# Performance work log

Hardware: AMD Instinct MI355X
Metric: run time of the kernel (lower is better)

Reference implementation:

```python
import jax, jax.numpy as jnp
import numpy as np

N_EMBD = 1024
N_HEAD = 16
HEAD = N_EMBD // N_HEAD


def setup_inputs() -> dict:
    key = jax.random.key(0)
    ks = jax.random.split(key, 5)
    B, T = 2, 2048
    s = 1.0 / np.sqrt(N_EMBD)
    return {
        "x": jax.random.normal(ks[0], (B, T, N_EMBD), dtype=jnp.float32),
        "w_attn": jax.random.normal(ks[1], (N_EMBD, 3 * N_EMBD), dtype=jnp.float32) * s,
        "b_attn": jnp.zeros((3 * N_EMBD,), dtype=jnp.float32),
        "w_proj": jax.random.normal(ks[2], (N_EMBD, N_EMBD), dtype=jnp.float32) * s,
        "b_proj": jnp.zeros((N_EMBD,), dtype=jnp.float32),
    }


def reference(x, w_attn, b_attn, w_proj, b_proj):
    B, T, C = x.shape
    qkv = x @ w_attn + b_attn                      # [B,T,3C]
    q, k, v = jnp.split(qkv, 3, axis=-1)
    def heads(t):
        return t.reshape(B, T, N_HEAD, HEAD).transpose(0, 2, 1, 3)  # [B,H,T,D]
    q, k, v = heads(q), heads(k), heads(v)
    scale = 1.0 / np.sqrt(HEAD).astype(np.float32)
    scores = jnp.einsum('bhqd,bhkd->bhqk', q, k) * scale
    causal = jnp.tril(jnp.ones((T, T), dtype=bool))
    scores = jnp.where(causal, scores, -jnp.inf)
    attn = jax.nn.softmax(scores, axis=-1)
    out = jnp.einsum('bhqk,bhkd->bhqd', attn, v)   # [B,H,T,D]
    out = out.transpose(0, 2, 1, 3).reshape(B, T, C)
    return out @ w_proj + b_proj
```

## Files before the change

### kernel.cpp

```cpp
#include <hip/hip_runtime.h>
#include <stdint.h>

#define N_EMBD 1024
#define N_HEADv 16
#define HEADv 64
#define Bv 2
#define Tv 2048
#define BT (Bv*Tv)
#define C3 (3*N_EMBD)

typedef __attribute__((ext_vector_type(8))) short bf16x8;
typedef __attribute__((ext_vector_type(4))) float f32x4;

typedef __attribute__((address_space(3))) uint32_t lds_u32;
typedef const __attribute__((address_space(1))) uint32_t glb_u32;

__device__ __forceinline__ void gload_lds16(const void* g, void* l){
  __builtin_amdgcn_global_load_lds((glb_u32*)g, (lds_u32*)l, 16, 0, 0);
}

__device__ __forceinline__ unsigned short f2bf(float f){
  union { float f; uint32_t u; } v; v.f = f;
  uint32_t u = v.u;
  uint32_t r = u + 0x7FFFu + ((u>>16)&1u);
  return (unsigned short)(r>>16);
}
__device__ __forceinline__ uint32_t f2bf_fast(float f){
  union { float f; uint32_t u; } v; v.f = f;
  return (v.u + 0x8000u) >> 16;
}
__device__ __forceinline__ float bf2f(unsigned short s){
  union { uint32_t u; float f; } v; v.u = ((uint32_t)s)<<16; return v.f;
}

__global__ void k_cvt_bf16(const float* __restrict__ in, unsigned short* __restrict__ out, long n){
  long i = ((long)blockIdx.x*blockDim.x + threadIdx.x)*8;
  if(i >= n) return;
  float4 a = *reinterpret_cast<const float4*>(in+i);
  float4 b = *reinterpret_cast<const float4*>(in+i+4);
  union { int4 v; unsigned short s[8]; } o;
  o.s[0]=f2bf(a.x); o.s[1]=f2bf(a.y); o.s[2]=f2bf(a.z); o.s[3]=f2bf(a.w);
  o.s[4]=f2bf(b.x); o.s[5]=f2bf(b.y); o.s[6]=f2bf(b.z); o.s[7]=f2bf(b.w);
  *reinterpret_cast<int4*>(out+i) = o.v;
}

__global__ void k_transpose_bf16(const float* __restrict__ in, unsigned short* __restrict__ out, int K, int N){
  __shared__ float tile[64][65];
  int n0 = blockIdx.x*64, k0 = blockIdx.y*64;
  int t = threadIdx.x;
  #pragma unroll
  for(int p=0;p<4;p++){
    int row = (t>>4) + p*16;
    int col4 = (t&15)*4;
    float4 v = *reinterpret_cast<const float4*>(&in[(size_t)(k0+row)*N + n0 + col4]);
    tile[row][col4+0]=v.x; tile[row][col4+1]=v.y; tile[row][col4+2]=v.z; tile[row][col4+3]=v.w;
  }
  __syncthreads();
  #pragma unroll
  for(int p=0;p<4;p++){
    int nrow = (t>>4) + p*16;
    int kc = (t&15)*4;
    ushort4 o;
    o.x = f2bf(tile[kc+0][nrow]);
    o.y = f2bf(tile[kc+1][nrow]);
    o.z = f2bf(tile[kc+2][nrow]);
    o.w = f2bf(tile[kc+3][nrow]);
    *reinterpret_cast<ushort4*>(&out[(size_t)(n0+nrow)*K + k0 + kc]) = o;
  }
}

template<int MODE>
__global__ __launch_bounds__(256) void k_gemm(
    const unsigned short* __restrict__ A,
    const unsigned short* __restrict__ Bt,
    const float* __restrict__ bias,
    void* __restrict__ Cout,
    int M, int N, int K)
{
  const int BK=64;
  const int TSZ=128*BK;
  __shared__ unsigned short As[2*TSZ];
  __shared__ unsigned short Bs[2*TSZ];
  int m0 = blockIdx.y*128, n0 = blockIdx.x*128;
  int t = threadIdx.x, lane = t&63, wid = t>>6;
  int wm = (wid>>1)*64, wn = (wid&1)*64;
  int g = lane>>4, r16 = lane&15;
  int rl  = lane>>3;
  int cle = (((lane&7) ^ rl) * 8);
  int rsw = r16 & 7;
  f32x4 acc[4][4] = {};

  #pragma unroll
  for(int c=0;c<4;c++){
    int rb = wid*32 + c*8;
    gload_lds16(&A [(size_t)(m0+rb+rl)*K + cle], &As[rb*BK]);
    gload_lds16(&Bt[(size_t)(n0+rb+rl)*K + cle], &Bs[rb*BK]);
  }
  __syncthreads();

  const int NIT = K/BK;
  for(int it=0; it<NIT; ++it){
    int cur = it & 1;
    if(it+1 < NIT){
      int k0 = (it+1)*BK;
      int nxt = (cur^1)*TSZ;
      #pragma unroll
      for(int c=0;c<4;c++){
        int rb = wid*32 + c*8;
        gload_lds16(&A [(size_t)(m0+rb+rl)*K + k0 + cle], &As[nxt + rb*BK]);
        gload_lds16(&Bt[(size_t)(n0+rb+rl)*K + k0 + cle], &Bs[nxt + rb*BK]);
      }
    }
    const unsigned short* Ab = &As[cur*TSZ];
    const unsigned short* Bb = &Bs[cur*TSZ];
    bf16x8 af[2][4], bfr[2][4];
    #pragma unroll
    for(int ks=0;ks<2;ks++){
      #pragma unroll
      for(int mi=0;mi<4;mi++)
        af[ks][mi]  = *reinterpret_cast<const bf16x8*>(&Ab[(wm+mi*16+r16)*BK + (((ks*4+g)^rsw)*8)]);
      #pragma unroll
      for(int ni=0;ni<4;ni++)
        bfr[ks][ni] = *reinterpret_cast<const bf16x8*>(&Bb[(wn+ni*16+r16)*BK + (((ks*4+g)^rsw)*8)]);
    }
    __builtin_amdgcn_s_setprio(1);
    #pragma unroll
    for(int ks=0;ks<2;ks++)
      #pragma unroll
      for(int mi=0;mi<4;mi++)
        #pragma unroll
        for(int ni=0;ni<4;ni++){
          if(MODE==0)
            acc[mi][ni] = __builtin_amdgcn_mfma_f32_16x16x32_bf16(af[ks][mi], bfr[ks][ni], acc[mi][ni], 0,0,0);
          else
            acc[mi][ni] = __builtin_amdgcn_mfma_f32_16x16x32_bf16(bfr[ks][ni], af[ks][mi], acc[mi][ni], 0,0,0);
        }
    __builtin_amdgcn_s_setprio(0);
    __syncthreads();
  }

  if(MODE==0){
    int which = (n0+wn)>>10;
    int h = ((n0+wn)&1023)>>6;
    int bb = m0>>11;
    int tt0 = (m0&2047) + wm;
    unsigned short* base = (unsigned short*)Cout;
    if(which < 2){
      float scale = (which==0) ? 0.18033688f : 1.0f;
      unsigned short* dst = base + (size_t)which*BT*N_EMBD
                          + (((size_t)bb*N_HEADv + h)*Tv + tt0)*HEADv;
      #pragma unroll
      for(int ni=0;ni<4;ni++){
        float bv = bias[n0+wn+ni*16+r16];
        int d = ni*16 + r16;
        #pragma unroll
        for(int mi=0;mi<4;mi++)
          #pragma unroll
          for(int reg=0;reg<4;reg++){
            int tt = mi*16 + g*4 + reg;
            dst[(size_t)tt*HEADv + d] = f2bf((acc[mi][ni][reg] + bv)*scale);
          }
      }
    } else {
      unsigned short* dst = base + 2ll*BT*N_EMBD
                          + (((size_t)bb*N_HEADv + h)*HEADv)*Tv + tt0;
      #pragma unroll
      for(int ni=0;ni<4;ni++){
        float bv = bias[n0+wn+ni*16+r16];
        int d = ni*16 + r16;
        #pragma unroll
        for(int mi=0;mi<4;mi++)
          #pragma unroll
          for(int reg=0;reg<4;reg++){
            int tt = mi*16 + g*4 + reg;
            dst[(size_t)d*Tv + tt] = f2bf(acc[mi][ni][reg] + bv);
          }
      }
    }
  } else {
    float* out = (float*)Cout;
    #pragma unroll
    for(int mi=0;mi<4;mi++){
      int m = m0+wm+mi*16+r16;
      #pragma unroll
      for(int ni=0;ni<4;ni++){
        int n = n0+wn+ni*16+g*4;
        float4 b4 = *reinterpret_cast<const float4*>(&bias[n]);
        float4 o4;
        o4.x = acc[mi][ni][0] + b4.x;
        o4.y = acc[mi][ni][1] + b4.y;
        o4.z = acc[mi][ni][2] + b4.z;
        o4.w = acc[mi][ni][3] + b4.w;
        *reinterpret_cast<float4*>(&out[(size_t)m*N + n]) = o4;
      }
    }
  }
}

__global__ __launch_bounds__(256) void k_attn(
    const unsigned short* __restrict__ QKV,
    unsigned short* __restrict__ O,
    unsigned short* __restrict__ partO,
    float2* __restrict__ stats)
{
  __shared__ unsigned short Ks[2][64][64];
  __shared__ unsigned short Vs[2][64][64];
  __shared__ unsigned short Ps[4][16][64];
  int blk = blockIdx.x;
  int bh = blk & 31;
  int j  = blk >> 5;
  int qt, kt0, ktN; bool single;
  if(j < 16)      { qt = 16+j;  kt0 = 0;  ktN = 16;    single = false; }
  else if(j < 32) { qt = 47-j;  kt0 = 16; ktN = qt+1;  single = false; }
  else            { qt = 47-j;  kt0 = 0;  ktN = qt+1;  single = true;  }

  int t = threadIdx.x, lane=t&63, wid=t>>6;
  int g = lane>>4, r16 = lane&15;
  const unsigned short* Qp  = QKV + (size_t)bh*Tv*HEADv;
  const unsigned short* Kp  = QKV + (size_t)BT*N_EMBD + (size_t)bh*Tv*HEADv;
  const unsigned short* Vtp = QKV + 2ll*BT*N_EMBD + (size_t)bh*HEADv*Tv;
  int q0 = qt*64 + wid*16;

  bf16x8 aq[2];
  #pragma unroll
  for(int kb=0;kb<2;kb++)
    aq[kb] = *reinterpret_cast<const bf16x8*>(&Qp[(size_t)(q0+r16)*HEADv + kb*32 + g*8]);

  const short ONE = (short)0x3F80;
  const bf16x8 ones8 = {ONE,ONE,ONE,ONE,ONE,ONE,ONE,ONE};

  f32x4 oacc[4] = {};
  f32x4 lacc = {};
  float m2 = 6.0f;

  int r0 = t>>3, c0 = (t&7)*8;
  int r1 = r0 + 32;
  int sw0 = c0 ^ ((r0&7)<<3);
  int sw1 = c0 ^ ((r1&7)<<3);
  int rsw = (r16&7)<<3;

  int4 kc0, kc1, vc0, vc1;
  kc0 = *reinterpret_cast<const int4*>(&Kp [(size_t)(kt0*64+r0)*HEADv + c0]);
  kc1 = *reinterpret_cast<const int4*>(&Kp [(size_t)(kt0*64+r1)*HEADv + c0]);
  vc0 = *reinterpret_cast<const int4*>(&Vtp[(size_t)r0*Tv + kt0*64 + c0]);
  vc1 = *reinterpret_cast<const int4*>(&Vtp[(size_t)r1*Tv + kt0*64 + c0]);
  *reinterpret_cast<int4*>(&Ks[0][r0][sw0]) = kc0;
  *reinterpret_cast<int4*>(&Ks[0][r1][sw1]) = kc1;
  *reinterpret_cast<int4*>(&Vs[0][r0][sw0]) = vc0;
  *reinterpret_cast<int4*>(&Vs[0][r1][sw1]) = vc1;
  if(ktN - kt0 > 1){
    kc0 = *reinterpret_cast<const int4*>(&Kp [(size_t)((kt0+1)*64+r0)*HEADv + c0]);
    kc1 = *reinterpret_cast<const int4*>(&Kp [(size_t)((kt0+1)*64+r1)*HEADv + c0]);
    vc0 = *reinterpret_cast<const int4*>(&Vtp[(size_t)r0*Tv + (kt0+1)*64 + c0]);
    vc1 = *reinterpret_cast<const int4*>(&Vtp[(size_t)r1*Tv + (kt0+1)*64 + c0]);
  }
  __syncthreads();

  for(int kt=kt0; kt<ktN; ++kt){
    int cur = kt & 1;
    if(kt+1 < ktN){
      *reinterpret_cast<int4*>(&Ks[cur^1][r0][sw0]) = kc0;
      *reinterpret_cast<int4*>(&Ks[cur^1][r1][sw1]) = kc1;
      *reinterpret_cast<int4*>(&Vs[cur^1][r0][sw0]) = vc0;
      *reinterpret_cast<int4*>(&Vs[cur^1][r1][sw1]) = vc1;
      if(kt+2 < ktN){
        kc0 = *reinterpret_cast<const int4*>(&Kp [(size_t)((kt+2)*64+r0)*HEADv + c0]);
        kc1 = *reinterpret_cast<const int4*>(&Kp [(size_t)((kt+2)*64+r1)*HEADv + c0]);
        vc0 = *reinterpret_cast<const int4*>(&Vtp[(size_t)r0*Tv + (kt+2)*64 + c0]);
        vc1 = *reinterpret_cast<const int4*>(&Vtp[(size_t)r1*Tv + (kt+2)*64 + c0]);
      }
    }

    f32x4 sacc[4];
    __builtin_amdgcn_s_setprio(1);
    #pragma unroll
    for(int nb=0;nb<4;nb++){
      sacc[nb] = (f32x4){0.f,0.f,0.f,0.f};
      #pragma unroll
      for(int kb=0;kb<2;kb++){
        bf16x8 bk = *reinterpret_cast<const bf16x8*>(&Ks[cur][nb*16+r16][(kb*32+g*8) ^ rsw]);
        sacc[nb] = __builtin_amdgcn_mfma_f32_16x16x32_bf16(bk, aq[kb], sacc[nb],0,0,0);
      }
    }
    __builtin_amdgcn_s_setprio(0);

    bool diag = (kt == qt);
    float sv[4][4], pv[4][4];
    #pragma unroll
    for(int nb=0;nb<4;nb++)
      #pragma unroll
      for(int reg=0;reg<4;reg++){
        float s = sacc[nb][reg];
        if(diag){
          int keyin = nb*16 + g*4 + reg;
          if(keyin > wid*16 + r16) s = -1e30f;
        }
        sv[nb][reg] = s;
      }
    #pragma unroll
    for(int nb=0;nb<4;nb++)
      #pragma unroll
      for(int reg=0;reg<4;reg++)
        pv[nb][reg] = __builtin_amdgcn_exp2f(sv[nb][reg] - m2);

    float mxnb[4];
    #pragma unroll
    for(int nb=0;nb<4;nb++)
      mxnb[nb] = fmaxf(fmaxf(sv[nb][0],sv[nb][1]), fmaxf(sv[nb][2],sv[nb][3]));
    float mx = fmaxf(fmaxf(mxnb[0],mxnb[1]), fmaxf(mxnb[2],mxnb[3]));
    mx = fmaxf(mx, __shfl_xor(mx, 16, 64));
    mx = fmaxf(mx, __shfl_xor(mx, 32, 64));

    if(!__all(mx - m2 <= 11.5f)){
      float mn = fmaxf(m2, mx);
      float alpha = __builtin_amdgcn_exp2f(m2 - mn);
      lacc[0]*=alpha; lacc[1]*=alpha; lacc[2]*=alpha; lacc[3]*=alpha;
      #pragma unroll
      for(int nb=0;nb<4;nb++)
        #pragma unroll
        for(int reg=0;reg<4;reg++) oacc[nb][reg] *= alpha;
      m2 = mn;
      #pragma unroll
      for(int nb=0;nb<4;nb++)
        #pragma unroll
        for(int reg=0;reg<4;reg++)
          pv[nb][reg] = __builtin_amdgcn_exp2f(sv[nb][reg] - m2);
    }

    #pragma unroll
    for(int nb=0;nb<4;nb++){
      union { uint32_t u[2]; int2 v; } w;
      w.u[0] = f2bf_fast(pv[nb][0]) | (f2bf_fast(pv[nb][1])<<16);
      w.u[1] = f2bf_fast(pv[nb][2]) | (f2bf_fast(pv[nb][3])<<16);
      *reinterpret_cast<int2*>(&Ps[wid][r16][(nb*16+g*4) ^ rsw]) = w.v;
    }

    __builtin_amdgcn_s_setprio(1);
    #pragma unroll
    for(int kb=0;kb<2;kb++){
      bf16x8 ap = *reinterpret_cast<const bf16x8*>(&Ps[wid][r16][(kb*32+g*8) ^ rsw]);
      lacc = __builtin_amdgcn_mfma_f32_16x16x32_bf16(ones8, ap, lacc,0,0,0);
      #pragma unroll
      for(int nb=0;nb<4;nb++){
        bf16x8 bv = *reinterpret_cast<const bf16x8*>(&Vs[cur][nb*16+r16][(kb*32+g*8) ^ rsw]);
        oacc[nb] = __builtin_amdgcn_mfma_f32_16x16x32_bf16(bv, ap, oacc[nb],0,0,0);
      }
    }
    __builtin_amdgcn_s_setprio(0);
    __syncthreads();
  }

  float l = lacc[0];
  float rinv = 1.0f / l;
  if(single){
    int b = bh >> 4, h = bh & 15;
    size_t row = (size_t)b*Tv + q0 + r16;
    #pragma unroll
    for(int nb=0;nb<4;nb++){
      ushort4 o;
      o.x = f2bf(oacc[nb][0]*rinv);
      o.y = f2bf(oacc[nb][1]*rinv);
      o.z = f2bf(oacc[nb][2]*rinv);
      o.w = f2bf(oacc[nb][3]*rinv);
      *reinterpret_cast<ushort4*>(&O[row*N_EMBD + h*HEADv + nb*16 + g*4]) = o;
    }
  } else {
    int part = j*32 + bh;
    unsigned short* po = partO + (size_t)part*4096;
    int qloc = wid*16 + r16;
    #pragma unroll
    for(int nb=0;nb<4;nb++){
      ushort4 o;
      o.x = f2bf(oacc[nb][0]*rinv);
      o.y = f2bf(oacc[nb][1]*rinv);
      o.z = f2bf(oacc[nb][2]*rinv);
      o.w = f2bf(oacc[nb][3]*rinv);
      *reinterpret_cast<ushort4*>(&po[qloc*64 + nb*16 + g*4]) = o;
    }
    if(g==0) stats[part*64 + qloc] = make_float2(m2, l);
  }
}

__global__ __launch_bounds__(256) void k_merge(
    const unsigned short* __restrict__ partO,
    const float2* __restrict__ stats,
    unsigned short* __restrict__ O)
{
  int blk = blockIdx.x;
  int bh = blk & 31, qt = 16 + (blk >> 5);
  int p0 = (qt-16)*32 + bh;
  int p1 = (47-qt)*32 + bh;
  int t = threadIdx.x;
  int q = t >> 2, d0 = (t&3)*16;
  float2 s0 = stats[p0*64 + q];
  float2 s1 = stats[p1*64 + q];
  float m = fmaxf(s0.x, s1.x);
  float w0 = s0.y * __builtin_amdgcn_exp2f(s0.x - m);
  float w1 = s1.y * __builtin_amdgcn_exp2f(s1.x - m);
  float rinv = 1.f/(w0+w1);
  w0 *= rinv; w1 *= rinv;
  const unsigned short* a = partO + (size_t)p0*4096 + q*64 + d0;
  const unsigned short* b = partO + (size_t)p1*4096 + q*64 + d0;
  int bb = bh >> 4, h = bh & 15;
  unsigned short* o = O + ((size_t)bb*Tv + qt*64 + q)*N_EMBD + h*HEADv + d0;
  #pragma unroll
  for(int half=0; half<2; ++half){
    union { int4 v; unsigned short s[8]; } ua, ub, uo;
    ua.v = *reinterpret_cast<const int4*>(a + half*8);
    ub.v = *reinterpret_cast<const int4*>(b + half*8);
    #pragma unroll
    for(int e=0;e<8;e++)
      uo.s[e] = f2bf(bf2f(ua.s[e])*w0 + bf2f(ub.s[e])*w1);
    *reinterpret_cast<int4*>(o + half*8) = uo.v;
  }
}

extern "C" void kernel_launch(void* const* d_in, const int* in_sizes, int n_in,
                              void* d_out, int out_size, void* d_ws, size_t ws_size,
                              hipStream_t stream){
  const float* x      = (const float*)d_in[0];
  const float* w_attn = (const float*)d_in[1];
  const float* b_attn = (const float*)d_in[2];
  const float* w_proj = (const float*)d_in[3];
  const float* b_proj = (const float*)d_in[4];
  char* ws = (char*)d_ws;
  unsigned short* xb  = (unsigned short*)ws;
  unsigned short* qkv = (unsigned short*)(ws + 8ll*1024*1024);
  unsigned short* ob  = (unsigned short*)(ws + 32ll*1024*1024);
  unsigned short* wat = (unsigned short*)(ws + 40ll*1024*1024);
  unsigned short* wpt = (unsigned short*)(ws + 46ll*1024*1024);
  unsigned short* partO = xb;
  float2*        stats  = (float2*)wat;

  k_cvt_bf16<<<2048,256,0,stream>>>(x, xb, (long)BT*N_EMBD);
  k_transpose_bf16<<<dim3(C3/64, N_EMBD/64),256,0,stream>>>(w_attn, wat, N_EMBD, C3);
  k_transpose_bf16<<<dim3(N_EMBD/64, N_EMBD/64),256,0,stream>>>(w_proj, wpt, N_EMBD, N_EMBD);
  k_gemm<0><<<dim3(C3/128, BT/128),256,0,stream>>>(xb, wat, b_attn, (void*)qkv, BT, C3, N_EMBD);
  k_attn<<<dim3(48*32),256,0,stream>>>(qkv, ob, partO, stats);
  k_merge<<<dim3(512),256,0,stream>>>(partO, stats, ob);
  k_gemm<1><<<dim3(N_EMBD/128, BT/128),256,0,stream>>>(ob, wpt, b_proj, d_out, BT, N_EMBD, N_EMBD);
}
```

Measured before the change: 121.4 us.

## Halve GEMM K-tile and remap blocks XCD-aware with 1D grid

The GEMM K-tile drops from 64 to 32, which halves LDS use per block and should allow more resident blocks, with the swizzle and load mapping changed to match. The 2D grid becomes a 1D grid whose block index is permuted modulo 8, so consecutive tiles land on the same XCD and can share L2. The cost is twice as many loop iterations and barriers per K, with fewer MFMAs between syncs. The m/n decode hardcodes 32 row tiles (BT/128), which holds for both GEMMs.

Measured after the change: 136.5 us. 1.12x slower.

```diff
diff --git a/kernel.cpp b/kernel.cpp
--- a/kernel.cpp
+++ b/kernel.cpp
@@ -77,24 +77,26 @@
     void* __restrict__ Cout,
     int M, int N, int K)
 {
-  const int BK=64;
+  const int BK=32;
   const int TSZ=128*BK;
   __shared__ unsigned short As[2*TSZ];
   __shared__ unsigned short Bs[2*TSZ];
-  int m0 = blockIdx.y*128, n0 = blockIdx.x*128;
+  int bpx = gridDim.x >> 3;
+  int wgid = (blockIdx.x & 7)*bpx + (blockIdx.x >> 3);
+  int m0 = (wgid & 31)*128, n0 = (wgid >> 5)*128;
   int t = threadIdx.x, lane = t&63, wid = t>>6;
   int wm = (wid>>1)*64, wn = (wid&1)*64;
   int g = lane>>4, r16 = lane&15;
-  int rl  = lane>>3;
-  int cle = (((lane&7) ^ rl) * 8);
-  int rsw = r16 & 7;
+  int rl  = lane>>2;
+  int scol = ((lane&3) ^ (rl&3))*8;
+  int rk = r16 & 3;
   f32x4 acc[4][4] = {};
 
   #pragma unroll
-  for(int c=0;c<4;c++){
-    int rb = wid*32 + c*8;
-    gload_lds16(&A [(size_t)(m0+rb+rl)*K + cle], &As[rb*BK]);
-    gload_lds16(&Bt[(size_t)(n0+rb+rl)*K + cle], &Bs[rb*BK]);
+  for(int c=0;c<2;c++){
+    int rb = wid*16 + c*64;
+    gload_lds16(&A [(size_t)(m0+rb+rl)*K + scol], &As[rb*BK]);
+    gload_lds16(&Bt[(size_t)(n0+rb+rl)*K + scol], &Bs[rb*BK]);
   }
   __syncthreads();
 
@@ -105,36 +107,31 @@
       int k0 = (it+1)*BK;
       int nxt = (cur^1)*TSZ;
       #pragma unroll
-      for(int c=0;c<4;c++){
-        int rb = wid*32 + c*8;
-        gload_lds16(&A [(size_t)(m0+rb+rl)*K + k0 + cle], &As[nxt + rb*BK]);
-        gload_lds16(&Bt[(size_t)(n0+rb+rl)*K + k0 + cle], &Bs[nxt + rb*BK]);
+      for(int c=0;c<2;c++){
+        int rb = wid*16 + c*64;
+        gload_lds16(&A [(size_t)(m0+rb+rl)*K + k0 + scol], &As[nxt + rb*BK]);
+        gload_lds16(&Bt[(size_t)(n0+rb+rl)*K + k0 + scol], &Bs[nxt + rb*BK]);
       }
     }
     const unsigned short* Ab = &As[cur*TSZ];
     const unsigned short* Bb = &Bs[cur*TSZ];
-    bf16x8 af[2][4], bfr[2][4];
-    #pragma unroll
-    for(int ks=0;ks<2;ks++){
-      #pragma unroll
-      for(int mi=0;mi<4;mi++)
-        af[ks][mi]  = *reinterpret_cast<const bf16x8*>(&Ab[(wm+mi*16+r16)*BK + (((ks*4+g)^rsw)*8)]);
-      #pragma unroll
-      for(int ni=0;ni<4;ni++)
-        bfr[ks][ni] = *reinterpret_cast<const bf16x8*>(&Bb[(wn+ni*16+r16)*BK + (((ks*4+g)^rsw)*8)]);
-    }
+    bf16x8 af[4], bfr[4];
+    #pragma unroll
+    for(int mi=0;mi<4;mi++)
+      af[mi]  = *reinterpret_cast<const bf16x8*>(&Ab[(wm+mi*16+r16)*BK + ((g^rk)*8)]);
+    #pragma unroll
+    for(int ni=0;ni<4;ni++)
+      bfr[ni] = *reinterpret_cast<const bf16x8*>(&Bb[(wn+ni*16+r16)*BK + ((g^rk)*8)]);
     __builtin_amdgcn_s_setprio(1);
     #pragma unroll
-    for(int ks=0;ks<2;ks++)
-      #pragma unroll
-      for(int mi=0;mi<4;mi++)
-        #pragma unroll
-        for(int ni=0;ni<4;ni++){
-          if(MODE==0)
-            acc[mi][ni] = __builtin_amdgcn_mfma_f32_16x16x32_bf16(af[ks][mi], bfr[ks][ni], acc[mi][ni], 0,0,0);
-          else
-            acc[mi][ni] = __builtin_amdgcn_mfma_f32_16x16x32_bf16(bfr[ks][ni], af[ks][mi], acc[mi][ni], 0,0,0);
-        }
+    for(int mi=0;mi<4;mi++)
+      #pragma unroll
+      for(int ni=0;ni<4;ni++){
+        if(MODE==0)
+          acc[mi][ni] = __builtin_amdgcn_mfma_f32_16x16x32_bf16(af[mi], bfr[ni], acc[mi][ni], 0,0,0);
+        else
+          acc[mi][ni] = __builtin_amdgcn_mfma_f32_16x16x32_bf16(bfr[ni], af[mi], acc[mi][ni], 0,0,0);
+      }
     __builtin_amdgcn_s_setprio(0);
     __syncthreads();
   }
@@ -435,8 +432,8 @@
   k_cvt_bf16<<<2048,256,0,stream>>>(x, xb, (long)BT*N_EMBD);
   k_transpose_bf16<<<dim3(C3/64, N_EMBD/64),256,0,stream>>>(w_attn, wat, N_EMBD, C3);
   k_transpose_bf16<<<dim3(N_EMBD/64, N_EMBD/64),256,0,stream>>>(w_proj, wpt, N_EMBD, N_EMBD);
-  k_gemm<0><<<dim3(C3/128, BT/128),256,0,stream>>>(xb, wat, b_attn, (void*)qkv, BT, C3, N_EMBD);
+  k_gemm<0><<<dim3((C3/128)*(BT/128)),256,0,stream>>>(xb, wat, b_attn, (void*)qkv, BT, C3, N_EMBD);
   k_attn<<<dim3(48*32),256,0,stream>>>(qkv, ob, partO, stats);
   k_merge<<<dim3(512),256,0,stream>>>(partO, stats, ob);
-  k_gemm<1><<<dim3(N_EMBD/128, BT/128),256,0,stream>>>(ob, wpt, b_proj, d_out, BT, N_EMBD, N_EMBD);
-}
+  k_gemm<1><<<dim3((N_EMBD/128)*(BT/128)),256,0,stream>>>(ob, wpt, b_proj, d_out, BT, N_EMBD, N_EMBD);
+}
```
